# Kernel optimization log

Hardware: AMD Instinct MI355X
Metric: run time of the kernel (lower is better)

## Reference

```python
import jax, jax.numpy as jnp
import numpy as np

NUM_LAYERS = 16
IN_SIZE = 1024
OUT_SIZE = 1024
B, S = 64, 128

def setup_inputs() -> dict:
    key = jax.random.key(0)
    k1, k2, k3 = jax.random.split(key, 3)
    x = jax.random.normal(k1, (B, S, IN_SIZE), dtype=jnp.float32)
    layer_idx = jax.random.randint(k2, (S,), 0, NUM_LAYERS)
    weight = jax.random.normal(k3, (NUM_LAYERS, OUT_SIZE, IN_SIZE), dtype=jnp.float32)
    return {"x": x, "layer_idx": layer_idx, "weight": weight}

def reference(x, layer_idx, weight):
    # Branch: layer_idx is 1D with len == S (per-position weight selection).
    # Gather per-position weights [S, O, D] and do one batched contraction,
    # equivalent to the Python loop of per-step matmuls in the original.
    w = weight[layer_idx]                       # [S, O, D]
    out = jnp.einsum('bsd,sod->bso', x, w)      # [B, S, O]
    return out
```

## Files before the change

### kernel.cpp

```cpp
#include <hip/hip_runtime.h>
#include <hip/hip_bf16.h>

#define B_ 64
#define S_ 128
#define D_ 1024
#define O_ 1024
#define L_ 16

typedef __bf16 bf16x8 __attribute__((ext_vector_type(8)));
typedef float f32x4 __attribute__((ext_vector_type(4)));

#define WS_W   0ull
#define WS_X   33554432ull
#define WS_P   50331648ull
#define WS_NEED (50331664ull + 72ull * 16ull)

__device__ __forceinline__ unsigned f2bf2(float a, float b) {
    union { float f; unsigned u; } x{a}, y{b};
    unsigned lo = x.u + 0x7FFFu + ((x.u >> 16) & 1u);
    unsigned hi = y.u + 0x7FFFu + ((y.u >> 16) & 1u);
    return (lo >> 16) | (hi & 0xFFFF0000u);
}

__device__ __forceinline__ void gload16(const void* g, void* l) {
    __builtin_amdgcn_global_load_lds(
        (const __attribute__((address_space(1))) void*)g,
        (__attribute__((address_space(3))) void*)l, 16, 0, 0);
}

__global__ __launch_bounds__(256) void moshi_convert(
    const float* __restrict__ x, const float* __restrict__ w,
    const int* __restrict__ lidx, unsigned char* __restrict__ ws) {
    if (blockIdx.x == 0 && threadIdx.x < 16) {
        int t = threadIdx.x;
        int cnt[16];
        #pragma unroll 1
        for (int m = 0; m < 16; ++m) cnt[m] = 0;
        for (int s = 0; s < S_; ++s) ++cnt[lidx[s]];
        int off = 0;
        for (int m = 0; m < t; ++m) off += (cnt[m] + 1) >> 1;
        int4* pairs = (int4*)(ws + WS_P + 16);
        int k = 0, prev = -1;
        for (int s = 0; s < S_; ++s) {
            if (lidx[s] == t) {
                if (k & 1) pairs[off + (k >> 1)] = make_int4(prev, s, t, 0);
                prev = s; ++k;
            }
        }
        if (k & 1) pairs[off + (k >> 1)] = make_int4(prev, prev, t, 0);
        if (t == 0) {
            int tot = 0;
            for (int m = 0; m < 16; ++m) tot += (cnt[m] + 1) >> 1;
            *(int*)(ws + WS_P) = tot;
        }
    }
    const int TW = L_ * O_ * D_ / 4;
    const int TX = B_ * S_ * D_ / 4;
    for (int f = blockIdx.x * 256 + threadIdx.x; f < TW + TX; f += gridDim.x * 256) {
        if (f < TW) {
            const float4 v = *reinterpret_cast<const float4*>(w + 4ull * f);
            uint2 pk = { f2bf2(v.x, v.y), f2bf2(v.z, v.w) };
            int d4 = f & 255, o = (f >> 8) & 1023, l = f >> 18;
            int nt = o >> 7, row = o & 127, kt = d4 >> 4;
            unsigned byte = ((unsigned)((l * 8 + nt) * 16 + kt)) * 16384u
                          + (((unsigned)(row * 128 + (d4 & 15) * 8)) ^ ((row & 7) << 4));
            *reinterpret_cast<uint2*>(ws + WS_W + byte) = pk;
        } else {
            int g = f - TW;
            const float4 v = *reinterpret_cast<const float4*>(x + 4ull * g);
            uint2 pk = { f2bf2(v.x, v.y), f2bf2(v.z, v.w) };
            int d4 = g & 255, s = (g >> 8) & 127, b = g >> 15;
            int kt = d4 >> 4;
            unsigned byte = ((unsigned)(s * 16 + kt)) * 8192u
                          + (((unsigned)(b * 128 + (d4 & 15) * 8)) ^ ((b & 7) << 4));
            *reinterpret_cast<uint2*>(ws + WS_X + byte) = pk;
        }
    }
}

__global__ __launch_bounds__(256) void moshi_gemm_paired(
    const unsigned char* __restrict__ ws, float* __restrict__ out) {
    __shared__ __align__(16) unsigned char lw[2][16384];
    __shared__ __align__(16) unsigned char lx[2][16384];

    const int bid = (blockIdx.x & 7) * 72 + (blockIdx.x >> 3);
    const int pi = bid >> 3;
    const int nt = bid & 7;
    const int np = *reinterpret_cast<const int*>(ws + WS_P);
    if (pi >= np) return;
    const int4 pr = *reinterpret_cast<const int4*>(ws + WS_P + 16 + 16ull * pi);
    const int s0 = pr.x, s1 = pr.y, l = pr.z;

    const unsigned char* wt  = ws + WS_W + ((size_t)(l * 8 + nt) * 16) * 16384;
    const unsigned char* xt0 = ws + WS_X + (size_t)s0 * 16 * 8192;
    const unsigned char* xt1 = ws + WS_X + (size_t)s1 * 16 * 8192;

    const int tid = threadIdx.x, lane = tid & 63, wid = tid >> 6;
    const int wm = wid >> 1, wn = wid & 1;
    const int swz = (lane & 7) << 4;
    const int kb  = (lane >> 4) << 4;
    const int a_base = (wm * 64 + (lane & 15)) * 128 + kb;
    const int b_base = (wn * 64 + (lane & 15)) * 128 + kb;

    f32x4 acc[4][4];
    #pragma unroll
    for (int i = 0; i < 4; ++i)
        #pragma unroll
        for (int j = 0; j < 4; ++j)
            acc[i][j] = (f32x4)0.0f;

    auto STAGE = [&](int kt, int b) {
        #pragma unroll
        for (int p = 0; p < 4; ++p)
            gload16(wt + (size_t)kt * 16384 + tid * 16 + p * 4096,
                    &lw[b][tid * 16 + p * 4096]);
        gload16(xt0 + (size_t)kt * 8192 + tid * 16,        &lx[b][tid * 16]);
        gload16(xt0 + (size_t)kt * 8192 + tid * 16 + 4096, &lx[b][tid * 16 + 4096]);
        gload16(xt1 + (size_t)kt * 8192 + tid * 16,        &lx[b][8192 + tid * 16]);
        gload16(xt1 + (size_t)kt * 8192 + tid * 16 + 4096, &lx[b][8192 + tid * 16 + 4096]);
    };

    STAGE(0, 0);
    __syncthreads();

    #pragma unroll 1
    for (int kt = 0; kt < 16; ++kt) {
        const int cur = kt & 1;
        if (kt < 15) STAGE(kt + 1, cur ^ 1);
        const unsigned char* lxb = lx[cur];
        const unsigned char* lwb = lw[cur];
        #pragma unroll
        for (int kk = 0; kk < 2; ++kk) {
            bf16x8 af[4], bf[4];
            #pragma unroll
            for (int mi = 0; mi < 4; ++mi)
                af[mi] = *reinterpret_cast<const bf16x8*>(
                    lxb + (((a_base + kk * 64) ^ swz) + mi * 2048));
            #pragma unroll
            for (int ni = 0; ni < 4; ++ni)
                bf[ni] = *reinterpret_cast<const bf16x8*>(
                    lwb + (((b_base + kk * 64) ^ swz) + ni * 2048));
            #pragma unroll
            for (int mi = 0; mi < 4; ++mi)
                #pragma unroll
                for (int ni = 0; ni < 4; ++ni)
                    acc[mi][ni] = __builtin_amdgcn_mfma_f32_16x16x32_bf16(
                        af[mi], bf[ni], acc[mi][ni], 0, 0, 0);
        }
        __syncthreads();
    }

    const int s_sel = wm ? s1 : s0;
    const int col0 = nt * 128 + wn * 64 + (lane & 15);
    const int r0 = (lane >> 4) << 2;
    #pragma unroll
    for (int mi = 0; mi < 4; ++mi)
        #pragma unroll
        for (int ni = 0; ni < 4; ++ni)
            #pragma unroll
            for (int r = 0; r < 4; ++r) {
                int b = mi * 16 + r0 + r;
                out[((size_t)b * S_ + s_sel) * O_ + col0 + ni * 16] = acc[mi][ni][r];
            }
}

__global__ __launch_bounds__(256) void moshi_flin_fallback(
    const float* __restrict__ x, const int* __restrict__ lidx,
    const float* __restrict__ w, float* __restrict__ out) {
    __shared__ __align__(16) unsigned char lxs[64 * 128];
    __shared__ __align__(16) unsigned char lws[128 * 128];
    const int bid = blockIdx.x;
    const int s = bid >> 3, n0 = (bid & 7) << 7;
    const int tid = threadIdx.x, lane = tid & 63, wid = tid >> 6;
    const int idx = lidx[s];
    const float* wb = w + (size_t)idx * O_ * D_ + (size_t)n0 * D_;
    const float* xb = x + (size_t)s * D_;
    const int swz = (lane & 7) << 4;
    const int kb = (lane >> 4) << 4;
    const int a_base = (lane & 15) * 128 + kb;
    const int b_base = (wid * 32 + (lane & 15)) * 128 + kb;
    f32x4 acc[4][2];
    #pragma unroll
    for (int i = 0; i < 4; ++i)
        #pragma unroll
        for (int j = 0; j < 2; ++j) acc[i][j] = (f32x4)0.0f;
    for (int kt = 0; kt < D_; kt += 64) {
        __syncthreads();
        #pragma unroll
        for (int p = 0; p < 4; ++p) {
            int f = tid + p * 256, row = f >> 4, c = (f & 15) << 2;
            const float4 v = *reinterpret_cast<const float4*>(
                xb + (size_t)row * (S_ * D_) + kt + c);
            uint2 pk = { f2bf2(v.x, v.y), f2bf2(v.z, v.w) };
            *reinterpret_cast<uint2*>(&lxs[(row * 128 + c * 2) ^ ((row & 7) << 4)]) = pk;
        }
        #pragma unroll
        for (int p = 0; p < 8; ++p) {
            int f = tid + p * 256, row = f >> 4, c = (f & 15) << 2;
            const float4 v = *reinterpret_cast<const float4*>(
                wb + (size_t)row * D_ + kt + c);
            uint2 pk = { f2bf2(v.x, v.y), f2bf2(v.z, v.w) };
            *reinterpret_cast<uint2*>(&lws[(row * 128 + c * 2) ^ ((row & 7) << 4)]) = pk;
        }
        __syncthreads();
        #pragma unroll
        for (int kk = 0; kk < 2; ++kk) {
            bf16x8 af[4], bfr[2];
            #pragma unroll
            for (int mi = 0; mi < 4; ++mi)
                af[mi] = *reinterpret_cast<const bf16x8*>(
                    &lxs[(((a_base + kk * 64) ^ swz) + mi * 2048)]);
            #pragma unroll
            for (int ni = 0; ni < 2; ++ni)
                bfr[ni] = *reinterpret_cast<const bf16x8*>(
                    &lws[(((b_base + kk * 64) ^ swz) + ni * 2048)]);
            #pragma unroll
            for (int mi = 0; mi < 4; ++mi)
                #pragma unroll
                for (int ni = 0; ni < 2; ++ni)
                    acc[mi][ni] = __builtin_amdgcn_mfma_f32_16x16x32_bf16(
                        af[mi], bfr[ni], acc[mi][ni], 0, 0, 0);
        }
    }
    float* ob = out + (size_t)s * O_ + n0 + wid * 32 + (lane & 15);
    const int r0 = (lane >> 4) << 2;
    #pragma unroll
    for (int mi = 0; mi < 4; ++mi)
        #pragma unroll
        for (int ni = 0; ni < 2; ++ni)
            #pragma unroll
            for (int r = 0; r < 4; ++r) {
                int b = mi * 16 + r0 + r;
                ob[(size_t)b * (S_ * O_) + ni * 16] = acc[mi][ni][r];
            }
}

extern "C" void kernel_launch(void* const* d_in, const int* in_sizes, int n_in,
                              void* d_out, int out_size, void* d_ws, size_t ws_size,
                              hipStream_t stream) {
    const float* x  = (const float*)d_in[0];
    const int* lidx = (const int*)d_in[1];
    const float* w  = (const float*)d_in[2];
    float* out      = (float*)d_out;

    if (ws_size < WS_NEED) {
        moshi_flin_fallback<<<dim3(128 * 8), dim3(256), 0, stream>>>(x, lidx, w, out);
        return;
    }
    unsigned char* ws = (unsigned char*)d_ws;
    moshi_convert<<<dim3(4096), dim3(256), 0, stream>>>(x, w, lidx, ws);
    moshi_gemm_paired<<<dim3(72 * 8), dim3(256), 0, stream>>>(ws, out);
}
```

Measured before the change: 66.06 us.

## Widen convert stores to 16B per thread and use 512-thread single-buffered GEMM

Measured after the change: 58.91 us. 10.8% less time.

```diff
diff --git a/kernel.cpp b/kernel.cpp
--- a/kernel.cpp
+++ b/kernel.cpp
@@ -9,6 +9,7 @@
 
 typedef __bf16 bf16x8 __attribute__((ext_vector_type(8)));
 typedef float f32x4 __attribute__((ext_vector_type(4)));
+typedef unsigned u32x4 __attribute__((ext_vector_type(4)));
 
 #define WS_W   0ull
 #define WS_X   33554432ull
@@ -54,34 +55,45 @@
             *(int*)(ws + WS_P) = tot;
         }
     }
-    const int TW = L_ * O_ * D_ / 4;
-    const int TX = B_ * S_ * D_ / 4;
-    for (int f = blockIdx.x * 256 + threadIdx.x; f < TW + TX; f += gridDim.x * 256) {
-        if (f < TW) {
-            const float4 v = *reinterpret_cast<const float4*>(w + 4ull * f);
-            uint2 pk = { f2bf2(v.x, v.y), f2bf2(v.z, v.w) };
-            int d4 = f & 255, o = (f >> 8) & 1023, l = f >> 18;
-            int nt = o >> 7, row = o & 127, kt = d4 >> 4;
-            unsigned byte = ((unsigned)((l * 8 + nt) * 16 + kt)) * 16384u
-                          + (((unsigned)(row * 128 + (d4 & 15) * 8)) ^ ((row & 7) << 4));
-            *reinterpret_cast<uint2*>(ws + WS_W + byte) = pk;
-        } else {
-            int g = f - TW;
-            const float4 v = *reinterpret_cast<const float4*>(x + 4ull * g);
-            uint2 pk = { f2bf2(v.x, v.y), f2bf2(v.z, v.w) };
-            int d4 = g & 255, s = (g >> 8) & 127, b = g >> 15;
-            int kt = d4 >> 4;
-            unsigned byte = ((unsigned)(s * 16 + kt)) * 8192u
-                          + (((unsigned)(b * 128 + (d4 & 15) * 8)) ^ ((b & 7) << 4));
-            *reinterpret_cast<uint2*>(ws + WS_X + byte) = pk;
-        }
-    }
-}
-
-__global__ __launch_bounds__(256) void moshi_gemm_paired(
+    const int TW4 = L_ * O_ * D_ / 16;
+    const int t0 = blockIdx.x * 256 + threadIdx.x;
+    if (t0 < TW4) {
+        const float4* src = reinterpret_cast<const float4*>(w) + 4ull * t0;
+        float4 v0 = src[0], v1 = src[1], v2 = src[2], v3 = src[3];
+        u32x4 lo = { f2bf2(v0.x, v0.y), f2bf2(v0.z, v0.w),
+                     f2bf2(v1.x, v1.y), f2bf2(v1.z, v1.w) };
+        u32x4 hi = { f2bf2(v2.x, v2.y), f2bf2(v2.z, v2.w),
+                     f2bf2(v3.x, v3.y), f2bf2(v3.z, v3.w) };
+        int f = t0 * 4;
+        int d4 = f & 255, o = (f >> 8) & 1023, l = f >> 18;
+        int nt = o >> 7, row = o & 127, kt = d4 >> 4;
+        unsigned base = ((unsigned)((l * 8 + nt) * 16 + kt)) * 16384u + (unsigned)(row * 128);
+        unsigned c = (unsigned)((d4 & 15) * 8);
+        unsigned k = (unsigned)((row & 7) << 4);
+        *reinterpret_cast<u32x4*>(ws + WS_W + base + (c ^ k))        = lo;
+        *reinterpret_cast<u32x4*>(ws + WS_W + base + ((c + 16) ^ k)) = hi;
+    } else {
+        int g = (t0 - TW4) * 4;
+        const float4* src = reinterpret_cast<const float4*>(x) + 4ull * (t0 - TW4);
+        float4 v0 = src[0], v1 = src[1], v2 = src[2], v3 = src[3];
+        u32x4 lo = { f2bf2(v0.x, v0.y), f2bf2(v0.z, v0.w),
+                     f2bf2(v1.x, v1.y), f2bf2(v1.z, v1.w) };
+        u32x4 hi = { f2bf2(v2.x, v2.y), f2bf2(v2.z, v2.w),
+                     f2bf2(v3.x, v3.y), f2bf2(v3.z, v3.w) };
+        int d4 = g & 255, s = (g >> 8) & 127, b = g >> 15;
+        int kt = d4 >> 4;
+        unsigned base = ((unsigned)(s * 16 + kt)) * 8192u + (unsigned)(b * 128);
+        unsigned c = (unsigned)((d4 & 15) * 8);
+        unsigned k = (unsigned)((b & 7) << 4);
+        *reinterpret_cast<u32x4*>(ws + WS_X + base + (c ^ k))        = lo;
+        *reinterpret_cast<u32x4*>(ws + WS_X + base + ((c + 16) ^ k)) = hi;
+    }
+}
+
+__global__ __launch_bounds__(512) void moshi_gemm_n128(
     const unsigned char* __restrict__ ws, float* __restrict__ out) {
-    __shared__ __align__(16) unsigned char lw[2][16384];
-    __shared__ __align__(16) unsigned char lx[2][16384];
+    __shared__ __align__(16) unsigned char lw[16384];
+    __shared__ __align__(16) unsigned char lx[16384];
 
     const int bid = (blockIdx.x & 7) * 72 + (blockIdx.x >> 3);
     const int pi = bid >> 3;
@@ -96,67 +108,53 @@
     const unsigned char* xt1 = ws + WS_X + (size_t)s1 * 16 * 8192;
 
     const int tid = threadIdx.x, lane = tid & 63, wid = tid >> 6;
-    const int wm = wid >> 1, wn = wid & 1;
+    const int wm = wid >> 2, wn = wid & 3;
     const int swz = (lane & 7) << 4;
     const int kb  = (lane >> 4) << 4;
     const int a_base = (wm * 64 + (lane & 15)) * 128 + kb;
-    const int b_base = (wn * 64 + (lane & 15)) * 128 + kb;
-
-    f32x4 acc[4][4];
+    const int b_base = (wn * 32 + (lane & 15)) * 128 + kb;
+
+    f32x4 acc[4][2];
     #pragma unroll
     for (int i = 0; i < 4; ++i)
         #pragma unroll
-        for (int j = 0; j < 4; ++j)
-            acc[i][j] = (f32x4)0.0f;
-
-    auto STAGE = [&](int kt, int b) {
-        #pragma unroll
-        for (int p = 0; p < 4; ++p)
-            gload16(wt + (size_t)kt * 16384 + tid * 16 + p * 4096,
-                    &lw[b][tid * 16 + p * 4096]);
-        gload16(xt0 + (size_t)kt * 8192 + tid * 16,        &lx[b][tid * 16]);
-        gload16(xt0 + (size_t)kt * 8192 + tid * 16 + 4096, &lx[b][tid * 16 + 4096]);
-        gload16(xt1 + (size_t)kt * 8192 + tid * 16,        &lx[b][8192 + tid * 16]);
-        gload16(xt1 + (size_t)kt * 8192 + tid * 16 + 4096, &lx[b][8192 + tid * 16 + 4096]);
-    };
-
-    STAGE(0, 0);
-    __syncthreads();
+        for (int j = 0; j < 2; ++j) acc[i][j] = (f32x4)0.0f;
 
     #pragma unroll 1
     for (int kt = 0; kt < 16; ++kt) {
-        const int cur = kt & 1;
-        if (kt < 15) STAGE(kt + 1, cur ^ 1);
-        const unsigned char* lxb = lx[cur];
-        const unsigned char* lwb = lw[cur];
+        __syncthreads();
+        gload16(wt  + (size_t)kt * 16384 + tid * 16,        lw + tid * 16);
+        gload16(wt  + (size_t)kt * 16384 + tid * 16 + 8192, lw + tid * 16 + 8192);
+        gload16(xt0 + (size_t)kt * 8192  + tid * 16,        lx + tid * 16);
+        gload16(xt1 + (size_t)kt * 8192  + tid * 16,        lx + tid * 16 + 8192);
+        __syncthreads();
         #pragma unroll
         for (int kk = 0; kk < 2; ++kk) {
-            bf16x8 af[4], bf[4];
+            bf16x8 af[4], bfr[2];
             #pragma unroll
             for (int mi = 0; mi < 4; ++mi)
                 af[mi] = *reinterpret_cast<const bf16x8*>(
-                    lxb + (((a_base + kk * 64) ^ swz) + mi * 2048));
-            #pragma unroll
-            for (int ni = 0; ni < 4; ++ni)
-                bf[ni] = *reinterpret_cast<const bf16x8*>(
-                    lwb + (((b_base + kk * 64) ^ swz) + ni * 2048));
+                    lx + (((a_base + kk * 64) ^ swz) + mi * 2048));
+            #pragma unroll
+            for (int ni = 0; ni < 2; ++ni)
+                bfr[ni] = *reinterpret_cast<const bf16x8*>(
+                    lw + (((b_base + kk * 64) ^ swz) + ni * 2048));
             #pragma unroll
             for (int mi = 0; mi < 4; ++mi)
                 #pragma unroll
-                for (int ni = 0; ni < 4; ++ni)
+                for (int ni = 0; ni < 2; ++ni)
                     acc[mi][ni] = __builtin_amdgcn_mfma_f32_16x16x32_bf16(
-                        af[mi], bf[ni], acc[mi][ni], 0, 0, 0);
-        }
-        __syncthreads();
+                        af[mi], bfr[ni], acc[mi][ni], 0, 0, 0);
+        }
     }
 
     const int s_sel = wm ? s1 : s0;
-    const int col0 = nt * 128 + wn * 64 + (lane & 15);
+    const int col0 = nt * 128 + wn * 32 + (lane & 15);
     const int r0 = (lane >> 4) << 2;
     #pragma unroll
     for (int mi = 0; mi < 4; ++mi)
         #pragma unroll
-        for (int ni = 0; ni < 4; ++ni)
+        for (int ni = 0; ni < 2; ++ni)
             #pragma unroll
             for (int r = 0; r < 4; ++r) {
                 int b = mi * 16 + r0 + r;
@@ -188,19 +186,19 @@
         __syncthreads();
         #pragma unroll
         for (int p = 0; p < 4; ++p) {
-            int f = tid + p * 256, row = f >> 4, c = (f & 15) << 2;
+            int f = tid + p * 256, row = f >> 4, cc = (f & 15) << 2;
             const float4 v = *reinterpret_cast<const float4*>(
-                xb + (size_t)row * (S_ * D_) + kt + c);
+                xb + (size_t)row * (S_ * D_) + kt + cc);
             uint2 pk = { f2bf2(v.x, v.y), f2bf2(v.z, v.w) };
-            *reinterpret_cast<uint2*>(&lxs[(row * 128 + c * 2) ^ ((row & 7) << 4)]) = pk;
+            *reinterpret_cast<uint2*>(&lxs[(row * 128 + cc * 2) ^ ((row & 7) << 4)]) = pk;
         }
         #pragma unroll
         for (int p = 0; p < 8; ++p) {
-            int f = tid + p * 256, row = f >> 4, c = (f & 15) << 2;
+            int f = tid + p * 256, row = f >> 4, cc = (f & 15) << 2;
             const float4 v = *reinterpret_cast<const float4*>(
-                wb + (size_t)row * D_ + kt + c);
+                wb + (size_t)row * D_ + kt + cc);
             uint2 pk = { f2bf2(v.x, v.y), f2bf2(v.z, v.w) };
-            *reinterpret_cast<uint2*>(&lws[(row * 128 + c * 2) ^ ((row & 7) << 4)]) = pk;
+            *reinterpret_cast<uint2*>(&lws[(row * 128 + cc * 2) ^ ((row & 7) << 4)]) = pk;
         }
         __syncthreads();
         #pragma unroll
@@ -248,6 +246,6 @@
         return;
     }
     unsigned char* ws = (unsigned char*)d_ws;
-    moshi_convert<<<dim3(4096), dim3(256), 0, stream>>>(x, w, lidx, ws);
-    moshi_gemm_paired<<<dim3(72 * 8), dim3(256), 0, stream>>>(ws, out);
-}
+    moshi_convert<<<dim3(6144), dim3(256), 0, stream>>>(x, w, lidx, ws);
+    moshi_gemm_n128<<<dim3(72 * 8), dim3(512), 0, stream>>>(ws, out);
+}
```
